# Performance work log

Hardware: AMD Instinct MI355X
Metric: run time of the kernel (lower is better)

Reference implementation:

```python
import jax, jax.numpy as jnp
import numpy as np

B, N, D = 8, 2048, 512
S = 4096  # max_swaps


def setup_inputs() -> dict:
    key = jax.random.key(0)
    ks = jax.random.split(key, 5)
    h = jax.random.normal(ks[0], (B, N, D), dtype=jnp.float32)
    indices = jax.random.randint(ks[1], (B, S, 4), 0, N, dtype=jnp.int64)
    # MLP params (Linear stores weight as (out,in) in torch; we keep (in,out) and matmul)
    W1 = jax.random.normal(ks[2], (4 * D, D), dtype=jnp.float32) * (1.0 / np.sqrt(4 * D))
    b1 = jnp.zeros((D,), dtype=jnp.float32)
    W2 = jax.random.normal(ks[3], (D, D // 2), dtype=jnp.float32) * (1.0 / np.sqrt(D))
    b2 = jnp.zeros((D // 2,), dtype=jnp.float32)
    W3 = jax.random.normal(ks[4], (D // 2, 1), dtype=jnp.float32) * (1.0 / np.sqrt(D // 2))
    b3 = jnp.zeros((1,), dtype=jnp.float32)
    return {"h": h, "indices": indices, "W1": W1, "b1": b1, "W2": W2, "b2": b2, "W3": W3, "b3": b3}


def reference(h, indices, W1, b1, W2, b2, W3, b3):
    # h: (B, N, D); indices: (B, S, 4) node ids per swap
    swap_emb = jnp.take_along_axis(h[:, None, :, :], indices[..., None].astype(jnp.int32),
                                   axis=2)  # broadcast-gather -> (B, S, 4, D)
    # equivalently: h[batch_idx, indices]; implemented as per-batch gather
    swap_emb = jax.vmap(lambda hb, ib: hb[ib])(h, indices)  # (B, S, 4, D)
    swap_feats = swap_emb.reshape(h.shape[0], indices.shape[1], -1)  # (B, S, 4D)
    x = jax.nn.gelu(swap_feats @ W1 + b1, approximate=False)
    x = jax.nn.gelu(x @ W2 + b2, approximate=False)
    scores = (x @ W3 + b3)[..., 0]  # (B, S)
    rates = jax.nn.softplus(scores)
    return rates
```

## Files before the change

kernel.cpp:

```cpp
#include <hip/hip_runtime.h>
#include <math.h>

#define BATCH 8
#define NNODES 2048
#define DDIM 512
#define SWAPS 4096
#define M_TOTAL (BATCH * SWAPS)
#define KD DDIM
#define K2 DDIM
#define N2 (DDIM / 2)

typedef __attribute__((ext_vector_type(8))) __bf16 bf16x8;
typedef __attribute__((ext_vector_type(4))) float f32x4;
typedef __attribute__((ext_vector_type(8))) unsigned short us8;
typedef unsigned short ushort_t;

__device__ __forceinline__ float gelu_fast(float x) {
    const float u = 0.7978845608028654f * x * fmaf(0.044715f * x, x, 1.0f);
    const float e = __expf(-2.0f * fabsf(u));
    float t = (1.0f - e) / (1.0f + e);
    t = copysignf(t, u);
    return 0.5f * x * (1.0f + t);
}
__device__ __forceinline__ float softplus_f(float x) {
    return fmaxf(x, 0.0f) + log1pf(expf(-fabsf(x)));
}
__device__ __forceinline__ unsigned short f2bf(float f) {
    unsigned int u = __builtin_bit_cast(unsigned int, f);
    u += 0x7FFFu + ((u >> 16) & 1u);
    return (unsigned short)(u >> 16);
}
__device__ __forceinline__ float bf2f(unsigned short s) {
    return __builtin_bit_cast(float, (unsigned int)s << 16);
}
__device__ __forceinline__ void glds16(const void* g, void* l) {
    __builtin_amdgcn_global_load_lds(
        (const __attribute__((address_space(1))) void*)g,
        (__attribute__((address_space(3))) void*)l, 16, 0, 0);
}

__global__ __launch_bounds__(256) void convert_kernel(
    const float* __restrict__ h, const float* __restrict__ W1,
    const float* __restrict__ W2, ushort_t* __restrict__ h_bf,
    ushort_t* __restrict__ W1pt, ushort_t* __restrict__ W2f)
{
    const int bid = blockIdx.x;
    const int tid = threadIdx.x;
    if (bid < 4096) {
        const size_t i = ((size_t)bid * 256 + tid) * 8;
        float4 v0 = *(const float4*)(h + i);
        float4 v1 = *(const float4*)(h + i + 4);
        us8 o;
        o[0] = f2bf(v0.x); o[1] = f2bf(v0.y); o[2] = f2bf(v0.z); o[3] = f2bf(v0.w);
        o[4] = f2bf(v1.x); o[5] = f2bf(v1.y); o[6] = f2bf(v1.z); o[7] = f2bf(v1.w);
        *(us8*)(h_bf + i) = o;
    } else if (bid < 4096 + 256) {
        __shared__ ushort_t sT[64][72];
        const int tb = bid - 4096;
        const int kt = tb >> 3, nt = tb & 7;
        const int kl = tid >> 4;
        const int n4 = (tid & 15) * 4;
        #pragma unroll
        for (int p = 0; p < 4; ++p) {
            const int k_local = p * 16 + kl;
            float4 v = *(const float4*)(W1 + (size_t)(kt * 64 + k_local) * 512
                                        + nt * 64 + n4);
            sT[n4 + 0][k_local] = f2bf(v.x);
            sT[n4 + 1][k_local] = f2bf(v.y);
            sT[n4 + 2][k_local] = f2bf(v.z);
            sT[n4 + 3][k_local] = f2bf(v.w);
        }
        __syncthreads();
        const int n_local = tid >> 2, ch = tid & 3;
        const int j = (kt >> 3) * 512 + nt * 64 + n_local;
        const int d0 = (kt & 7) * 64 + ch * 16;
        us8 o0, o1;
        #pragma unroll
        for (int e = 0; e < 8; ++e) { o0[e] = sT[n_local][ch * 16 + e];
                                      o1[e] = sT[n_local][ch * 16 + 8 + e]; }
        *(us8*)(W1pt + (size_t)j * KD + d0)     = o0;
        *(us8*)(W1pt + (size_t)j * KD + d0 + 8) = o1;
    } else {
        size_t e = ((size_t)(bid - 4352) * 256 + tid) * 4;
        const int k = (int)(e >> 8), n = (int)(e & 255);
        const int kc = k >> 5, quad = (k >> 3) & 3, pos = k & 7;
        const size_t base = (size_t)kc * 8192 + quad * 8 + pos;
        float4 v = *(const float4*)(W2 + e);
        W2f[base + (size_t)(n + 0) * 32] = f2bf(v.x);
        W2f[base + (size_t)(n + 1) * 32] = f2bf(v.y);
        W2f[base + (size_t)(n + 2) * 32] = f2bf(v.z);
        W2f[base + (size_t)(n + 3) * 32] = f2bf(v.w);
    }
}

__global__ __launch_bounds__(256) void gemm1_dense(
    const ushort_t* __restrict__ h_bf, const ushort_t* __restrict__ W1pt,
    ushort_t* __restrict__ P2)
{
    __shared__ __align__(16) char smem[32768];

    const int tid = threadIdx.x;
    const int w = tid >> 6, lane = tid & 63;
    const int quad = lane >> 4, l16 = lane & 15;
    const int wr = w >> 1, wc = w & 1;

    const int bid = blockIdx.x;
    const int xcd = bid & 7;
    const int r = bid >> 3;
    const int m0 = xcd * NNODES + (r & 15) * 128;
    const int n0 = (r >> 4) * 128;

    const int row0 = tid >> 2, sub = tid & 3;
    const int cg = (sub - (row0 >> 1)) & 3;
    const ushort_t* bA0 = h_bf + (size_t)(m0 + row0) * KD + cg * 8;
    const ushort_t* bA1 = h_bf + (size_t)(m0 + row0 + 64) * KD + cg * 8;
    const ushort_t* bB0 = W1pt + (size_t)(n0 + row0) * KD + cg * 8;
    const ushort_t* bB1 = W1pt + (size_t)(n0 + row0 + 64) * KD + cg * 8;

    int pa[4], pb[4];
    #pragma unroll
    for (int i = 0; i < 4; ++i) {
        const int rA = wr * 64 + i * 16 + l16;
        const int rB = wc * 64 + i * 16 + l16;
        pa[i] = rA * 64 + (((quad + (rA >> 1)) & 3) * 16);
        pb[i] = 8192 + rB * 64 + (((quad + (rB >> 1)) & 3) * 16);
    }

    f32x4 acc[4][4] = {};

    auto stage = [&](int kt, int half) {
        const int oo = kt * 32;
        char* base = smem + half * 16384;
        glds16(bA0 + oo, base + w * 1024);
        glds16(bA1 + oo, base + 4096 + w * 1024);
        glds16(bB0 + oo, base + 8192 + w * 1024);
        glds16(bB1 + oo, base + 12288 + w * 1024);
    };
    auto compute = [&](int half) {
        const char* base = smem + half * 16384;
        bf16x8 af[4], bfr[4];
        #pragma unroll
        for (int i = 0; i < 4; ++i) {
            af[i]  = *(const bf16x8*)(base + pa[i]);
            bfr[i] = *(const bf16x8*)(base + pb[i]);
        }
        #pragma unroll
        for (int i = 0; i < 4; ++i)
            #pragma unroll
            for (int jj = 0; jj < 4; ++jj)
                acc[i][jj] = __builtin_amdgcn_mfma_f32_16x16x32_bf16(
                    af[i], bfr[jj], acc[i][jj], 0, 0, 0);
    };

    for (int kt = 0; kt < 16; kt += 2) {
        stage(kt, 0);
        stage(kt + 1, 1);
        __syncthreads();
        compute(0);
        compute(1);
        __syncthreads();
    }

    #pragma unroll
    for (int jj = 0; jj < 4; ++jj) {
        const int j = n0 + wc * 64 + jj * 16 + l16;
        const int sg = j >> 9, nh = j & 511;
        const size_t base = ((size_t)(xcd * 2 + (nh >> 8)) * NNODES) * 1024
                          + (size_t)(sg << 8) + (nh & 255);
        #pragma unroll
        for (int i = 0; i < 4; ++i) {
            f32x4 v = acc[i][jj];
            #pragma unroll
            for (int rr = 0; rr < 4; ++rr) {
                const int node = (m0 + wr * 64 + i * 16 + quad * 4 + rr) & (NNODES - 1);
                P2[base + (size_t)node * 1024] = f2bf(v[rr]);
            }
        }
    }
}

__global__ __launch_bounds__(512) void fused_tail(
    const ushort_t* __restrict__ P2, const int* __restrict__ idx,
    const float* __restrict__ b1, const ushort_t* __restrict__ W2f,
    const float* __restrict__ b2, const float* __restrict__ W3,
    const float* __restrict__ b3, float* __restrict__ out)
{
    __shared__ __align__(16) char smem[66560];

    const int tid = threadIdx.x;
    const int w = tid >> 6, lane = tid & 63;
    const int quad = lane >> 4, l16 = lane & 15;

    const int bid = blockIdx.x;
    const int b = bid & 7;
    const int m0 = b * SWAPS + (bid >> 3) * 64;

    {
        const int row = tid >> 3;
        const int ws  = tid & 7;
        const int ap  = ws & 3;
        const int ncs = ws >> 2;
        const int acg = (ap - (row >> 1)) & 3;
        const int4 iv = *(const int4*)(idx + (size_t)(m0 + row) * 4);
        const ushort_t* Pr = P2 + (size_t)(b * 2 + ncs) * NNODES * 1024;
        const ushort_t* p0 = Pr + (size_t)iv.x * 1024 + 0 * 256;
        const ushort_t* p1 = Pr + (size_t)iv.y * 1024 + 1 * 256;
        const ushort_t* p2 = Pr + (size_t)iv.z * 1024 + 2 * 256;
        const ushort_t* p3 = Pr + (size_t)iv.w * 1024 + 3 * 256;
        #pragma unroll 4
        for (int it = 0; it < 8; ++it) {
            const int kc = ncs * 8 + it;
            const int pos0 = it * 32 + acg * 8;
            us8 v0 = *(const us8*)(p0 + pos0);
            us8 v1 = *(const us8*)(p1 + pos0);
            us8 v2 = *(const us8*)(p2 + pos0);
            us8 v3 = *(const us8*)(p3 + pos0);
            const float* bp = b1 + ncs * 256 + pos0;
            float4 ba = *(const float4*)bp;
            float4 bb = *(const float4*)(bp + 4);
            float s[8] = { ba.x, ba.y, ba.z, ba.w, bb.x, bb.y, bb.z, bb.w };
            #pragma unroll
            for (int e = 0; e < 8; ++e)
                s[e] += bf2f(v0[e]) + bf2f(v1[e]) + bf2f(v2[e]) + bf2f(v3[e]);
            us8 o;
            #pragma unroll
            for (int e = 0; e < 8; ++e) o[e] = f2bf(gelu_fast(s[e]));
            *(us8*)(smem + kc * 4096 + row * 64 + ap * 16) = o;
        }
    }
    __syncthreads();

    const int rg = w >> 2, cg = w & 3;
    int paRow[2];
    #pragma unroll
    for (int i = 0; i < 2; ++i) {
        const int rA = rg * 32 + i * 16 + l16;
        paRow[i] = rA * 64 + (((quad + (rA >> 1)) & 3) * 16);
    }
    const ushort_t* Bbase = W2f + (size_t)(cg * 64 + l16) * 32 + quad * 8;

    f32x4 acc[2][4] = {};

    #pragma unroll 2
    for (int kc = 0; kc < 16; ++kc) {
        bf16x8 af0 = *(const bf16x8*)(smem + kc * 4096 + paRow[0]);
        bf16x8 af1 = *(const bf16x8*)(smem + kc * 4096 + paRow[1]);
        #pragma unroll
        for (int jf = 0; jf < 4; ++jf) {
            bf16x8 bfr = *(const bf16x8*)(Bbase + (size_t)kc * 8192 + jf * 512);
            acc[0][jf] = __builtin_amdgcn_mfma_f32_16x16x32_bf16(af0, bfr, acc[0][jf], 0, 0, 0);
            acc[1][jf] = __builtin_amdgcn_mfma_f32_16x16x32_bf16(af1, bfr, acc[1][jf], 0, 0, 0);
        }
    }

    float part[2][4] = {};
    #pragma unroll
    for (int jf = 0; jf < 4; ++jf) {
        const int n = cg * 64 + jf * 16 + l16;
        const float w3 = W3[n];
        const float bb2 = b2[n];
        #pragma unroll
        for (int i = 0; i < 2; ++i) {
            f32x4 v = acc[i][jf];
            #pragma unroll
            for (int rr = 0; rr < 4; ++rr)
                part[i][rr] = fmaf(gelu_fast(v[rr] + bb2), w3, part[i][rr]);
        }
    }
    #pragma unroll
    for (int off = 1; off < 16; off <<= 1)
        #pragma unroll
        for (int i = 0; i < 2; ++i)
            #pragma unroll
            for (int rr = 0; rr < 4; ++rr)
                part[i][rr] += __shfl_xor(part[i][rr], off);

    float* red = (float*)(smem + 65536);
    if (l16 == 0) {
        #pragma unroll
        for (int i = 0; i < 2; ++i)
            #pragma unroll
            for (int rr = 0; rr < 4; ++rr)
                red[cg * 64 + rg * 32 + i * 16 + quad * 4 + rr] = part[i][rr];
    }
    __syncthreads();
    if (tid < 64) {
        const float v = red[tid] + red[64 + tid] + red[128 + tid] + red[192 + tid];
        out[m0 + tid] = softplus_f(v + b3[0]);
    }
}

extern "C" void kernel_launch(void* const* d_in, const int* in_sizes, int n_in,
                              void* d_out, int out_size, void* d_ws, size_t ws_size,
                              hipStream_t stream) {
    const float* h   = (const float*)d_in[0];
    const int*   idx = (const int*)d_in[1];
    const float* W1  = (const float*)d_in[2];
    const float* b1  = (const float*)d_in[3];
    const float* W2  = (const float*)d_in[4];
    const float* b2  = (const float*)d_in[5];
    const float* W3  = (const float*)d_in[6];
    const float* b3  = (const float*)d_in[7];
    float* out = (float*)d_out;

    char* ws = (char*)d_ws;
    ushort_t* P2    = (ushort_t*)ws;
    ushort_t* h_bf  = (ushort_t*)(ws + (64u << 20));
    ushort_t* W1pt  = (ushort_t*)(ws + (80u << 20));
    ushort_t* W2f   = (ushort_t*)(ws + (82u << 20));

    convert_kernel<<<4480, 256, 0, stream>>>(h, W1, W2, h_bf, W1pt, W2f);
    gemm1_dense<<<2048, 256, 0, stream>>>(h_bf, W1pt, P2);
    fused_tail<<<512, 512, 0, stream>>>(P2, idx, b1, W2f, b2, W3, b3, out);
}
```

Measured before the change: 170.5 us.

## Merge convert, GEMM1 and tail into one persistent kernel with grid barriers

Replaces the three kernel launches with a single persistent kernel of 512 blocks that uses atomic-counter grid barriers between the conversion, dense GEMM and gather/MLP tail phases. Each block loops over several GEMM tiles and two tail sub-tiles, so the tail now runs at 256 threads with a smaller LDS footprint. The aim is to remove launch gaps and inter-kernel drain. The cost is spin-wait barriers, which need all 512 blocks co-resident, plus an extra memset per call, and the tail runs with fewer threads per block.

```diff
diff --git a/kernel.cpp b/kernel.cpp
--- a/kernel.cpp
+++ b/kernel.cpp
@@ -8,7 +8,7 @@
 #define M_TOTAL (BATCH * SWAPS)
 #define KD DDIM
 #define K2 DDIM
-#define N2 (DDIM / 2)
+#define NBLOCKS 512u
 
 typedef __attribute__((ext_vector_type(8))) __bf16 bf16x8;
 typedef __attribute__((ext_vector_type(4))) float f32x4;
@@ -39,254 +39,268 @@
         (__attribute__((address_space(3))) void*)l, 16, 0, 0);
 }
 
-__global__ __launch_bounds__(256) void convert_kernel(
-    const float* __restrict__ h, const float* __restrict__ W1,
-    const float* __restrict__ W2, ushort_t* __restrict__ h_bf,
-    ushort_t* __restrict__ W1pt, ushort_t* __restrict__ W2f)
+__device__ __forceinline__ void grid_barrier(unsigned int* ctr) {
+    __syncthreads();
+    __threadfence();
+    if (threadIdx.x == 0) {
+        atomicAdd(ctr, 1u);
+        while (atomicAdd(ctr, 0u) < NBLOCKS)
+            __builtin_amdgcn_s_sleep(8);
+    }
+    __syncthreads();
+    __threadfence();
+}
+
+__global__ __launch_bounds__(256, 2) void mega_kernel(
+    const float* __restrict__ h, const int* __restrict__ idx,
+    const float* __restrict__ W1, const float* __restrict__ b1,
+    const float* __restrict__ W2, const float* __restrict__ b2,
+    const float* __restrict__ W3, const float* __restrict__ b3,
+    ushort_t* __restrict__ h_bf, ushort_t* __restrict__ W1pt,
+    ushort_t* __restrict__ W2f, ushort_t* __restrict__ P2,
+    unsigned int* __restrict__ ctrs, float* __restrict__ out)
 {
+    __shared__ __align__(16) char smem[33280];
+
+    const int tid = threadIdx.x;
     const int bid = blockIdx.x;
-    const int tid = threadIdx.x;
-    if (bid < 4096) {
-        const size_t i = ((size_t)bid * 256 + tid) * 8;
-        float4 v0 = *(const float4*)(h + i);
-        float4 v1 = *(const float4*)(h + i + 4);
-        us8 o;
-        o[0] = f2bf(v0.x); o[1] = f2bf(v0.y); o[2] = f2bf(v0.z); o[3] = f2bf(v0.w);
-        o[4] = f2bf(v1.x); o[5] = f2bf(v1.y); o[6] = f2bf(v1.z); o[7] = f2bf(v1.w);
-        *(us8*)(h_bf + i) = o;
-    } else if (bid < 4096 + 256) {
-        __shared__ ushort_t sT[64][72];
-        const int tb = bid - 4096;
-        const int kt = tb >> 3, nt = tb & 7;
-        const int kl = tid >> 4;
-        const int n4 = (tid & 15) * 4;
-        #pragma unroll
-        for (int p = 0; p < 4; ++p) {
-            const int k_local = p * 16 + kl;
-            float4 v = *(const float4*)(W1 + (size_t)(kt * 64 + k_local) * 512
-                                        + nt * 64 + n4);
-            sT[n4 + 0][k_local] = f2bf(v.x);
-            sT[n4 + 1][k_local] = f2bf(v.y);
-            sT[n4 + 2][k_local] = f2bf(v.z);
-            sT[n4 + 3][k_local] = f2bf(v.w);
-        }
-        __syncthreads();
-        const int n_local = tid >> 2, ch = tid & 3;
-        const int j = (kt >> 3) * 512 + nt * 64 + n_local;
-        const int d0 = (kt & 7) * 64 + ch * 16;
-        us8 o0, o1;
-        #pragma unroll
-        for (int e = 0; e < 8; ++e) { o0[e] = sT[n_local][ch * 16 + e];
-                                      o1[e] = sT[n_local][ch * 16 + 8 + e]; }
-        *(us8*)(W1pt + (size_t)j * KD + d0)     = o0;
-        *(us8*)(W1pt + (size_t)j * KD + d0 + 8) = o1;
-    } else {
-        size_t e = ((size_t)(bid - 4352) * 256 + tid) * 4;
-        const int k = (int)(e >> 8), n = (int)(e & 255);
-        const int kc = k >> 5, quad = (k >> 3) & 3, pos = k & 7;
-        const size_t base = (size_t)kc * 8192 + quad * 8 + pos;
-        float4 v = *(const float4*)(W2 + e);
-        W2f[base + (size_t)(n + 0) * 32] = f2bf(v.x);
-        W2f[base + (size_t)(n + 1) * 32] = f2bf(v.y);
-        W2f[base + (size_t)(n + 2) * 32] = f2bf(v.z);
-        W2f[base + (size_t)(n + 3) * 32] = f2bf(v.w);
-    }
-}
-
-__global__ __launch_bounds__(256) void gemm1_dense(
-    const ushort_t* __restrict__ h_bf, const ushort_t* __restrict__ W1pt,
-    ushort_t* __restrict__ P2)
-{
-    __shared__ __align__(16) char smem[32768];
-
-    const int tid = threadIdx.x;
     const int w = tid >> 6, lane = tid & 63;
     const int quad = lane >> 4, l16 = lane & 15;
-    const int wr = w >> 1, wc = w & 1;
-
-    const int bid = blockIdx.x;
-    const int xcd = bid & 7;
-    const int r = bid >> 3;
-    const int m0 = xcd * NNODES + (r & 15) * 128;
-    const int n0 = (r >> 4) * 128;
-
-    const int row0 = tid >> 2, sub = tid & 3;
-    const int cg = (sub - (row0 >> 1)) & 3;
-    const ushort_t* bA0 = h_bf + (size_t)(m0 + row0) * KD + cg * 8;
-    const ushort_t* bA1 = h_bf + (size_t)(m0 + row0 + 64) * KD + cg * 8;
-    const ushort_t* bB0 = W1pt + (size_t)(n0 + row0) * KD + cg * 8;
-    const ushort_t* bB1 = W1pt + (size_t)(n0 + row0 + 64) * KD + cg * 8;
-
-    int pa[4], pb[4];
-    #pragma unroll
-    for (int i = 0; i < 4; ++i) {
-        const int rA = wr * 64 + i * 16 + l16;
-        const int rB = wc * 64 + i * 16 + l16;
-        pa[i] = rA * 64 + (((quad + (rA >> 1)) & 3) * 16);
-        pb[i] = 8192 + rB * 64 + (((quad + (rB >> 1)) & 3) * 16);
+
+    {
+        const size_t tbase = ((size_t)bid * 256 + tid) * 8;
+        #pragma unroll
+        for (int it = 0; it < 8; ++it) {
+            const size_t i = tbase + (size_t)it * 1048576;
+            float4 v0 = *(const float4*)(h + i);
+            float4 v1 = *(const float4*)(h + i + 4);
+            us8 o;
+            o[0] = f2bf(v0.x); o[1] = f2bf(v0.y); o[2] = f2bf(v0.z); o[3] = f2bf(v0.w);
+            o[4] = f2bf(v1.x); o[5] = f2bf(v1.y); o[6] = f2bf(v1.z); o[7] = f2bf(v1.w);
+            *(us8*)(h_bf + i) = o;
+        }
+        if (bid < 256) {
+            ushort_t (*sT)[72] = (ushort_t(*)[72])smem;
+            const int kt = bid >> 3, nt = bid & 7;
+            const int kl = tid >> 4;
+            const int n4 = (tid & 15) * 4;
+            #pragma unroll
+            for (int p = 0; p < 4; ++p) {
+                const int k_local = p * 16 + kl;
+                float4 v = *(const float4*)(W1 + (size_t)(kt * 64 + k_local) * 512
+                                            + nt * 64 + n4);
+                sT[n4 + 0][k_local] = f2bf(v.x);
+                sT[n4 + 1][k_local] = f2bf(v.y);
+                sT[n4 + 2][k_local] = f2bf(v.z);
+                sT[n4 + 3][k_local] = f2bf(v.w);
+            }
+            __syncthreads();
+            const int n_local = tid >> 2, ch = tid & 3;
+            const int j = (kt >> 3) * 512 + nt * 64 + n_local;
+            const int d0 = (kt & 7) * 64 + ch * 16;
+            us8 o0, o1;
+            #pragma unroll
+            for (int e = 0; e < 8; ++e) { o0[e] = sT[n_local][ch * 16 + e];
+                                          o1[e] = sT[n_local][ch * 16 + 8 + e]; }
+            *(us8*)(W1pt + (size_t)j * KD + d0)     = o0;
+            *(us8*)(W1pt + (size_t)j * KD + d0 + 8) = o1;
+        } else if (bid < 384) {
+            size_t e = ((size_t)(bid - 256) * 256 + tid) * 4;
+            const int k = (int)(e >> 8), n = (int)(e & 255);
+            const int kc = k >> 5, qd = (k >> 3) & 3, pos = k & 7;
+            const size_t base = (size_t)kc * 8192 + qd * 8 + pos;
+            float4 v = *(const float4*)(W2 + e);
+            W2f[base + (size_t)(n + 0) * 32] = f2bf(v.x);
+            W2f[base + (size_t)(n + 1) * 32] = f2bf(v.y);
+            W2f[base + (size_t)(n + 2) * 32] = f2bf(v.z);
+            W2f[base + (size_t)(n + 3) * 32] = f2bf(v.w);
+        }
     }
-
-    f32x4 acc[4][4] = {};
-
-    auto stage = [&](int kt, int half) {
-        const int oo = kt * 32;
-        char* base = smem + half * 16384;
-        glds16(bA0 + oo, base + w * 1024);
-        glds16(bA1 + oo, base + 4096 + w * 1024);
-        glds16(bB0 + oo, base + 8192 + w * 1024);
-        glds16(bB1 + oo, base + 12288 + w * 1024);
-    };
-    auto compute = [&](int half) {
-        const char* base = smem + half * 16384;
-        bf16x8 af[4], bfr[4];
+    grid_barrier(ctrs + 0);
+
+    {
+        const int wr = w >> 1, wc = w & 1;
+        const int row0 = tid >> 2, sub = tid & 3;
+        const int cgs = (sub - (row0 >> 1)) & 3;
+
+        int pa[4], pb[4];
         #pragma unroll
         for (int i = 0; i < 4; ++i) {
-            af[i]  = *(const bf16x8*)(base + pa[i]);
-            bfr[i] = *(const bf16x8*)(base + pb[i]);
-        }
-        #pragma unroll
-        for (int i = 0; i < 4; ++i)
-            #pragma unroll
-            for (int jj = 0; jj < 4; ++jj)
-                acc[i][jj] = __builtin_amdgcn_mfma_f32_16x16x32_bf16(
-                    af[i], bfr[jj], acc[i][jj], 0, 0, 0);
-    };
-
-    for (int kt = 0; kt < 16; kt += 2) {
-        stage(kt, 0);
-        stage(kt + 1, 1);
-        __syncthreads();
-        compute(0);
-        compute(1);
-        __syncthreads();
+            const int rA = wr * 64 + i * 16 + l16;
+            const int rB = wc * 64 + i * 16 + l16;
+            pa[i] = rA * 64 + (((quad + (rA >> 1)) & 3) * 16);
+            pb[i] = 8192 + rB * 64 + (((quad + (rB >> 1)) & 3) * 16);
+        }
+
+        for (int tt = 0; tt < 4; ++tt) {
+            const int lb = bid + tt * 512;
+            const int xcd = lb & 7;
+            const int r = lb >> 3;
+            const int m0 = xcd * NNODES + (r & 15) * 128;
+            const int n0 = (r >> 4) * 128;
+
+            const ushort_t* bA0 = h_bf + (size_t)(m0 + row0) * KD + cgs * 8;
+            const ushort_t* bA1 = h_bf + (size_t)(m0 + row0 + 64) * KD + cgs * 8;
+            const ushort_t* bB0 = W1pt + (size_t)(n0 + row0) * KD + cgs * 8;
+            const ushort_t* bB1 = W1pt + (size_t)(n0 + row0 + 64) * KD + cgs * 8;
+
+            f32x4 acc[4][4] = {};
+
+            auto stage = [&](int kt, int half) {
+                const int oo = kt * 32;
+                char* base = smem + half * 16384;
+                glds16(bA0 + oo, base + w * 1024);
+                glds16(bA1 + oo, base + 4096 + w * 1024);
+                glds16(bB0 + oo, base + 8192 + w * 1024);
+                glds16(bB1 + oo, base + 12288 + w * 1024);
+            };
+            auto compute = [&](int half) {
+                const char* base = smem + half * 16384;
+                bf16x8 af[4], bfr[4];
+                #pragma unroll
+                for (int i = 0; i < 4; ++i) {
+                    af[i]  = *(const bf16x8*)(base + pa[i]);
+                    bfr[i] = *(const bf16x8*)(base + pb[i]);
+                }
+                #pragma unroll
+                for (int i = 0; i < 4; ++i)
+                    #pragma unroll
+                    for (int jj = 0; jj < 4; ++jj)
+                        acc[i][jj] = __builtin_amdgcn_mfma_f32_16x16x32_bf16(
+                            af[i], bfr[jj], acc[i][jj], 0, 0, 0);
+            };
+
+            __syncthreads();
+            for (int kt = 0; kt < 16; kt += 2) {
+                stage(kt, 0);
+                stage(kt + 1, 1);
+                __syncthreads();
+                compute(0);
+                compute(1);
+                __syncthreads();
+            }
+
+            #pragma unroll
+            for (int jj = 0; jj < 4; ++jj) {
+                const int j = n0 + wc * 64 + jj * 16 + l16;
+                const int sg = j >> 9, nh = j & 511;
+                const size_t base = ((size_t)(xcd * 2 + (nh >> 8)) * NNODES) * 1024
+                                  + (size_t)(sg << 8) + (nh & 255);
+                #pragma unroll
+                for (int i = 0; i < 4; ++i) {
+                    f32x4 v = acc[i][jj];
+                    #pragma unroll
+                    for (int rr = 0; rr < 4; ++rr) {
+                        const int node = (m0 + wr * 64 + i * 16 + quad * 4 + rr)
+                                         & (NNODES - 1);
+                        P2[base + (size_t)node * 1024] = f2bf(v[rr]);
+                    }
+                }
+            }
+        }
     }
-
-    #pragma unroll
-    for (int jj = 0; jj < 4; ++jj) {
-        const int j = n0 + wc * 64 + jj * 16 + l16;
-        const int sg = j >> 9, nh = j & 511;
-        const size_t base = ((size_t)(xcd * 2 + (nh >> 8)) * NNODES) * 1024
-                          + (size_t)(sg << 8) + (nh & 255);
-        #pragma unroll
-        for (int i = 0; i < 4; ++i) {
-            f32x4 v = acc[i][jj];
-            #pragma unroll
-            for (int rr = 0; rr < 4; ++rr) {
-                const int node = (m0 + wr * 64 + i * 16 + quad * 4 + rr) & (NNODES - 1);
-                P2[base + (size_t)node * 1024] = f2bf(v[rr]);
-            }
-        }
-    }
-}
-
-__global__ __launch_bounds__(512) void fused_tail(
-    const ushort_t* __restrict__ P2, const int* __restrict__ idx,
-    const float* __restrict__ b1, const ushort_t* __restrict__ W2f,
-    const float* __restrict__ b2, const float* __restrict__ W3,
-    const float* __restrict__ b3, float* __restrict__ out)
-{
-    __shared__ __align__(16) char smem[66560];
-
-    const int tid = threadIdx.x;
-    const int w = tid >> 6, lane = tid & 63;
-    const int quad = lane >> 4, l16 = lane & 15;
-
-    const int bid = blockIdx.x;
-    const int b = bid & 7;
-    const int m0 = b * SWAPS + (bid >> 3) * 64;
+    grid_barrier(ctrs + 1);
 
     {
-        const int row = tid >> 3;
-        const int ws  = tid & 7;
-        const int ap  = ws & 3;
-        const int ncs = ws >> 2;
-        const int acg = (ap - (row >> 1)) & 3;
-        const int4 iv = *(const int4*)(idx + (size_t)(m0 + row) * 4);
-        const ushort_t* Pr = P2 + (size_t)(b * 2 + ncs) * NNODES * 1024;
-        const ushort_t* p0 = Pr + (size_t)iv.x * 1024 + 0 * 256;
-        const ushort_t* p1 = Pr + (size_t)iv.y * 1024 + 1 * 256;
-        const ushort_t* p2 = Pr + (size_t)iv.z * 1024 + 2 * 256;
-        const ushort_t* p3 = Pr + (size_t)iv.w * 1024 + 3 * 256;
-        #pragma unroll 4
-        for (int it = 0; it < 8; ++it) {
-            const int kc = ncs * 8 + it;
-            const int pos0 = it * 32 + acg * 8;
-            us8 v0 = *(const us8*)(p0 + pos0);
-            us8 v1 = *(const us8*)(p1 + pos0);
-            us8 v2 = *(const us8*)(p2 + pos0);
-            us8 v3 = *(const us8*)(p3 + pos0);
-            const float* bp = b1 + ncs * 256 + pos0;
-            float4 ba = *(const float4*)bp;
-            float4 bb = *(const float4*)(bp + 4);
-            float s[8] = { ba.x, ba.y, ba.z, ba.w, bb.x, bb.y, bb.z, bb.w };
-            #pragma unroll
-            for (int e = 0; e < 8; ++e)
-                s[e] += bf2f(v0[e]) + bf2f(v1[e]) + bf2f(v2[e]) + bf2f(v3[e]);
-            us8 o;
-            #pragma unroll
-            for (int e = 0; e < 8; ++e) o[e] = f2bf(gelu_fast(s[e]));
-            *(us8*)(smem + kc * 4096 + row * 64 + ap * 16) = o;
-        }
-    }
-    __syncthreads();
-
-    const int rg = w >> 2, cg = w & 3;
-    int paRow[2];
-    #pragma unroll
-    for (int i = 0; i < 2; ++i) {
-        const int rA = rg * 32 + i * 16 + l16;
-        paRow[i] = rA * 64 + (((quad + (rA >> 1)) & 3) * 16);
-    }
-    const ushort_t* Bbase = W2f + (size_t)(cg * 64 + l16) * 32 + quad * 8;
-
-    f32x4 acc[2][4] = {};
-
-    #pragma unroll 2
-    for (int kc = 0; kc < 16; ++kc) {
-        bf16x8 af0 = *(const bf16x8*)(smem + kc * 4096 + paRow[0]);
-        bf16x8 af1 = *(const bf16x8*)(smem + kc * 4096 + paRow[1]);
-        #pragma unroll
-        for (int jf = 0; jf < 4; ++jf) {
-            bf16x8 bfr = *(const bf16x8*)(Bbase + (size_t)kc * 8192 + jf * 512);
-            acc[0][jf] = __builtin_amdgcn_mfma_f32_16x16x32_bf16(af0, bfr, acc[0][jf], 0, 0, 0);
-            acc[1][jf] = __builtin_amdgcn_mfma_f32_16x16x32_bf16(af1, bfr, acc[1][jf], 0, 0, 0);
-        }
-    }
-
-    float part[2][4] = {};
-    #pragma unroll
-    for (int jf = 0; jf < 4; ++jf) {
-        const int n = cg * 64 + jf * 16 + l16;
-        const float w3 = W3[n];
-        const float bb2 = b2[n];
-        #pragma unroll
-        for (int i = 0; i < 2; ++i) {
-            f32x4 v = acc[i][jf];
-            #pragma unroll
-            for (int rr = 0; rr < 4; ++rr)
-                part[i][rr] = fmaf(gelu_fast(v[rr] + bb2), w3, part[i][rr]);
-        }
-    }
-    #pragma unroll
-    for (int off = 1; off < 16; off <<= 1)
-        #pragma unroll
-        for (int i = 0; i < 2; ++i)
-            #pragma unroll
-            for (int rr = 0; rr < 4; ++rr)
-                part[i][rr] += __shfl_xor(part[i][rr], off);
-
-    float* red = (float*)(smem + 65536);
-    if (l16 == 0) {
-        #pragma unroll
-        for (int i = 0; i < 2; ++i)
-            #pragma unroll
-            for (int rr = 0; rr < 4; ++rr)
-                red[cg * 64 + rg * 32 + i * 16 + quad * 4 + rr] = part[i][rr];
-    }
-    __syncthreads();
-    if (tid < 64) {
-        const float v = red[tid] + red[64 + tid] + red[128 + tid] + red[192 + tid];
-        out[m0 + tid] = softplus_f(v + b3[0]);
+        const int b = bid & 7;
+        float* red = (float*)(smem + 32768);
+
+        for (int it2 = 0; it2 < 2; ++it2) {
+            const int m0 = b * SWAPS + (bid >> 3) * 64 + it2 * 32;
+
+            {
+                const int row = tid >> 3;
+                const int ws  = tid & 7;
+                const int ap  = ws & 3;
+                const int ncs = ws >> 2;
+                const int acg = (ap - (row >> 1)) & 3;
+                const int4 iv = *(const int4*)(idx + (size_t)(m0 + row) * 4);
+                const ushort_t* Pr = P2 + (size_t)(b * 2 + ncs) * NNODES * 1024;
+                const ushort_t* p0 = Pr + (size_t)iv.x * 1024 + 0 * 256;
+                const ushort_t* p1 = Pr + (size_t)iv.y * 1024 + 1 * 256;
+                const ushort_t* p2 = Pr + (size_t)iv.z * 1024 + 2 * 256;
+                const ushort_t* p3 = Pr + (size_t)iv.w * 1024 + 3 * 256;
+                __syncthreads();
+                #pragma unroll 4
+                for (int it = 0; it < 8; ++it) {
+                    const int kc = ncs * 8 + it;
+                    const int pos0 = it * 32 + acg * 8;
+                    us8 v0 = *(const us8*)(p0 + pos0);
+                    us8 v1 = *(const us8*)(p1 + pos0);
+                    us8 v2 = *(const us8*)(p2 + pos0);
+                    us8 v3 = *(const us8*)(p3 + pos0);
+                    const float* bp = b1 + ncs * 256 + pos0;
+                    float4 ba = *(const float4*)bp;
+                    float4 bb = *(const float4*)(bp + 4);
+                    float s[8] = { ba.x, ba.y, ba.z, ba.w, bb.x, bb.y, bb.z, bb.w };
+                    #pragma unroll
+                    for (int e = 0; e < 8; ++e)
+                        s[e] += bf2f(v0[e]) + bf2f(v1[e]) + bf2f(v2[e]) + bf2f(v3[e]);
+                    us8 o;
+                    #pragma unroll
+                    for (int e = 0; e < 8; ++e) o[e] = f2bf(gelu_fast(s[e]));
+                    *(us8*)(smem + kc * 2048 + row * 64 + ap * 16) = o;
+                }
+            }
+            __syncthreads();
+
+            const int cgp = w;
+            int paRow[2];
+            #pragma unroll
+            for (int i = 0; i < 2; ++i) {
+                const int rA = i * 16 + l16;
+                paRow[i] = rA * 64 + (((quad + (rA >> 1)) & 3) * 16);
+            }
+            const ushort_t* Bbase = W2f + (size_t)(cgp * 64 + l16) * 32 + quad * 8;
+
+            f32x4 acc2[2][4] = {};
+            #pragma unroll 2
+            for (int kc = 0; kc < 16; ++kc) {
+                bf16x8 af0 = *(const bf16x8*)(smem + kc * 2048 + paRow[0]);
+                bf16x8 af1 = *(const bf16x8*)(smem + kc * 2048 + paRow[1]);
+                #pragma unroll
+                for (int jf = 0; jf < 4; ++jf) {
+                    bf16x8 bfr = *(const bf16x8*)(Bbase + (size_t)kc * 8192 + jf * 512);
+                    acc2[0][jf] = __builtin_amdgcn_mfma_f32_16x16x32_bf16(af0, bfr, acc2[0][jf], 0, 0, 0);
+                    acc2[1][jf] = __builtin_amdgcn_mfma_f32_16x16x32_bf16(af1, bfr, acc2[1][jf], 0, 0, 0);
+                }
+            }
+
+            float part[2][4] = {};
+            #pragma unroll
+            for (int jf = 0; jf < 4; ++jf) {
+                const int n = cgp * 64 + jf * 16 + l16;
+                const float w3 = W3[n];
+                const float bb2 = b2[n];
+                #pragma unroll
+                for (int i = 0; i < 2; ++i) {
+                    f32x4 v = acc2[i][jf];
+                    #pragma unroll
+                    for (int rr = 0; rr < 4; ++rr)
+                        part[i][rr] = fmaf(gelu_fast(v[rr] + bb2), w3, part[i][rr]);
+                }
+            }
+            #pragma unroll
+            for (int off = 1; off < 16; off <<= 1)
+                #pragma unroll
+                for (int i = 0; i < 2; ++i)
+                    #pragma unroll
+                    for (int rr = 0; rr < 4; ++rr)
+                        part[i][rr] += __shfl_xor(part[i][rr], off);
+
+            if (l16 == 0) {
+                #pragma unroll
+                for (int i = 0; i < 2; ++i)
+                    #pragma unroll
+                    for (int rr = 0; rr < 4; ++rr)
+                        red[cgp * 32 + i * 16 + quad * 4 + rr] = part[i][rr];
+            }
+            __syncthreads();
+            if (tid < 32) {
+                const float v = red[tid] + red[32 + tid] + red[64 + tid] + red[96 + tid];
+                out[m0 + tid] = softplus_f(v + b3[0]);
+            }
+        }
     }
 }
 
@@ -308,8 +322,9 @@
     ushort_t* h_bf  = (ushort_t*)(ws + (64u << 20));
     ushort_t* W1pt  = (ushort_t*)(ws + (80u << 20));
     ushort_t* W2f   = (ushort_t*)(ws + (82u << 20));
-
-    convert_kernel<<<4480, 256, 0, stream>>>(h, W1, W2, h_bf, W1pt, W2f);
-    gemm1_dense<<<2048, 256, 0, stream>>>(h_bf, W1pt, P2);
-    fused_tail<<<512, 512, 0, stream>>>(P2, idx, b1, W2f, b2, W3, b3, out);
-}
+    unsigned int* ctrs = (unsigned int*)(ws + (83u << 20));
+
+    hipMemsetAsync(ctrs, 0, 64, stream);
+    mega_kernel<<<NBLOCKS, 256, 0, stream>>>(h, idx, W1, b1, W2, b2, W3, b3,
+                                             h_bf, W1pt, W2f, P2, ctrs, out);
+}
```

Result: slower. 424.3 us (+148.8%).
